# Kernel tuning notes

Hardware: AMD Instinct MI355X
Metric: run time of the kernel (lower is better)

Reference implementation:

```python
import jax, jax.numpy as jnp
from jax import lax
import numpy as np


def _conv(x, w, b):
    y = lax.conv_general_dilated(x, w, (1, 1), 'VALID', dimension_numbers=('NCHW', 'OIHW', 'NCHW'))
    return y + b[None, :, None, None]


def _prelu(x, a):
    return jnp.where(x > 0, x, a[None, :, None, None] * x)


def _pnet(x, c1w, c1b, p1, c2w, c2b, p2, c3w, c3b, p3, w41, b41, w42, b42):
    x = _prelu(_conv(x, c1w, c1b), p1)
    H, W = x.shape[2], x.shape[3]
    # MaxPool2d(2,2, ceil_mode=True): pad bottom/right with -inf when odd
    x = lax.reduce_window(x, -jnp.inf, lax.max, (1, 1, 2, 2), (1, 1, 2, 2),
                          ((0, 0), (0, 0), (0, H % 2), (0, W % 2)))
    x = _prelu(_conv(x, c2w, c2b), p2)
    x = _prelu(_conv(x, c3w, c3b), p3)
    a = jax.nn.softmax(_conv(x, w41, b41), axis=1)
    b = _conv(x, w42, b42)
    return b, a


def _nms(boxes, scores, imgidx, valid, thr):
    # masked, fixed-size batched NMS (per-image via coordinate offset trick)
    N = boxes.shape[0]
    order = jnp.argsort(-jnp.where(valid, scores, -1e9))
    b = boxes[order] + imgidx[order].astype(boxes.dtype)[:, None] * 1e5
    v = valid[order]
    x1, y1, x2, y2 = b[:, 0], b[:, 1], b[:, 2], b[:, 3]
    area = jnp.maximum(x2 - x1, 0.0) * jnp.maximum(y2 - y1, 0.0)
    ar = jnp.arange(N)

    def body(i, keep):
        iw = jnp.maximum(jnp.minimum(x2[i], x2) - jnp.maximum(x1[i], x1), 0.0)
        ih = jnp.maximum(jnp.minimum(y2[i], y2) - jnp.maximum(y1[i], y1), 0.0)
        inter = iw * ih
        iou = inter / (area[i] + area - inter + 1e-9)
        return keep & ~((iou > thr) & (ar > i) & keep[i])

    keep = lax.fori_loop(0, N, body, v)
    return order, keep


def _detect(images, c1w, c1b, p1, c2w, c2b, p2, c3w, c3b, p3, w41, b41, w42, b42):
    params = (c1w, c1b, p1, c2w, c2b, p2, c3w, c3b, p3, w41, b41, w42, b42)
    x = jnp.transpose(images, (0, 3, 1, 2))  # NHWC -> NCHW
    B, _, H, W = x.shape
    m = 12.0 / 20.0  # 12 / minsize
    scales = []
    ml, si = min(H, W) * m, m
    while ml >= 12:
        scales.append(si)
        si *= 0.709
        ml *= 0.709
    KS, THR0 = 512, 0.6  # fixed per-scale candidate capacity
    all_b, all_i, all_k = [], [], []
    for scale in scales:
        nh, nw = int(H * scale + 1), int(W * scale + 1)
        im = jax.image.resize(x, (B, 3, nh, nw), method='linear')
        im = (im - 127.5) * 0.0078125
        reg, label = _pnet(im, *params)
        probs = label[:, 1]  # [B,h,w]
        b_, h_, w_ = probs.shape
        yy, xx = jnp.meshgrid(jnp.arange(h_), jnp.arange(w_), indexing='ij')
        bbx = jnp.tile(xx.reshape(-1), b_).astype(x.dtype)
        bby = jnp.tile(yy.reshape(-1), b_).astype(x.dtype)
        # stride=2, cellsize=12 grid-cell -> image-space boxes
        q = [jnp.floor((2 * bbx + 1) / scale), jnp.floor((2 * bby + 1) / scale),
             jnp.floor((2 * bbx + 12) / scale), jnp.floor((2 * bby + 12) / scale)]
        score = probs.reshape(-1)
        reg4 = jnp.transpose(reg, (0, 2, 3, 1)).reshape(-1, 4)
        boxes9 = jnp.concatenate([jnp.stack(q + [score], axis=1), reg4], axis=1)  # [N,9]
        imgidx = jnp.repeat(jnp.arange(b_), h_ * w_)
        k = min(KS, boxes9.shape[0])
        vals, idx = lax.top_k(jnp.where(score >= THR0, score, -1e9), k)
        bsel, isel, vsel = boxes9[idx], imgidx[idx], vals > -1e8
        order, keep = _nms(bsel[:, :4], bsel[:, 4], isel, vsel, 0.5)
        all_b.append(bsel[order])
        all_i.append(isel[order])
        all_k.append(keep)
    boxes = jnp.concatenate(all_b, 0)
    iidx = jnp.concatenate(all_i, 0)
    kp = jnp.concatenate(all_k, 0)
    K2 = min(1024, boxes.shape[0])
    vals, idx = lax.top_k(jnp.where(kp, boxes[:, 4], -1e9), K2)
    b2, i2, v2 = boxes[idx], iidx[idx], vals > -1e8
    order, keep = _nms(b2[:, :4], b2[:, 4], i2, v2, 0.7)
    b2 = b2[order]
    regw, regh = b2[:, 2] - b2[:, 0], b2[:, 3] - b2[:, 1]
    out = jnp.stack([b2[:, 0] + b2[:, 5] * regw, b2[:, 1] + b2[:, 6] * regh,
                     b2[:, 2] + b2[:, 7] * regw, b2[:, 3] + b2[:, 8] * regh, b2[:, 4]], axis=1)
    # rerec: square-ify
    hh, ww = out[:, 3] - out[:, 1], out[:, 2] - out[:, 0]
    l = jnp.maximum(hh, ww)
    x1 = out[:, 0] + ww * 0.5 - l * 0.5
    y1 = out[:, 1] + hh * 0.5 - l * 0.5
    out = jnp.stack([x1, y1, x1 + l, y1 + l, out[:, 4]], axis=1)
    return out * keep[:, None].astype(out.dtype)  # invalid/suppressed rows zeroed


def setup_inputs():
    key = jax.random.key(0)
    ks = jax.random.split(key, 16)
    rn = lambda k, s, sc=0.1: jax.random.normal(k, s, dtype=jnp.float32) * sc
    return {
        'images': jax.random.uniform(ks[0], (8, 768, 768, 3), dtype=jnp.float32) * 255.0,
        'c1w': rn(ks[1], (10, 3, 3, 3)), 'c1b': rn(ks[2], (10,)),
        'p1': 0.25 * jnp.ones((10,), jnp.float32),
        'c2w': rn(ks[3], (16, 10, 3, 3)), 'c2b': rn(ks[4], (16,)),
        'p2': 0.25 * jnp.ones((16,), jnp.float32),
        'c3w': rn(ks[5], (32, 16, 3, 3)), 'c3b': rn(ks[6], (32,)),
        'p3': 0.25 * jnp.ones((32,), jnp.float32),
        'w41': rn(ks[7], (2, 32, 1, 1)), 'b41': rn(ks[8], (2,)),
        'w42': rn(ks[9], (4, 32, 1, 1)), 'b42': rn(ks[10], (4,)),
    }


def reference(images, c1w, c1b, p1, c2w, c2b, p2, c3w, c3b, p3, w41, b41, w42, b42):
    return _detect(images, c1w, c1b, p1, c2w, c2b, p2, c3w, c3b, p3, w41, b41, w42, b42)
```

## Files before the change

kernel.cpp:

```cpp
#include <hip/hip_runtime.h>
#include <stdint.h>

typedef unsigned long long u64;
typedef unsigned int u32;

#define TPB 256
#define NJMAX 12
#define NSC 11

__device__ __forceinline__ int findJob(const int* cum, int nj, int v) {
  int j = 0;
  while (j + 1 < nj && v >= cum[j + 1]) ++j;
  return j;
}

struct MkP { int ns; int nw[NSC]; float invs[NSC], ks[NSC];
             int oxB[NSC], T[NSC], wOff[NSC]; };

__global__ void k_mkweights(int* __restrict__ tX0, int* __restrict__ tCNT,
                            float* __restrict__ tWT, float* __restrict__ tW, MkP P) {
  const int s = blockIdx.x;
  const int nw = P.nw[s];
  const float invs = P.invs[s], ks = P.ks[s];
  const int T = P.T[s];
  for (int ox = threadIdx.x; ox < nw; ox += TPB) {
    float sx = ((float)ox + 0.5f) * invs - 0.5f;
    int x0 = (int)ceilf(sx - ks); if (x0 < 0) x0 = 0;
    int x1 = (int)floorf(sx + ks); if (x1 > 767) x1 = 767;
    float wt = 0.f;
    float* wv = tW + P.wOff[s];
    for (int j = x0; j <= x1; ++j) {
      float w = fmaxf(0.f, 1.f - fabsf(sx - (float)j) / ks);
      wt += w;
      wv[(j - x0) * nw + ox] = w;
    }
    for (int k = x1 - x0 + 1; k < T; ++k) wv[k * nw + ox] = 0.f;
    int g = P.oxB[s] + ox;
    tX0[g] = x0; tCNT[g] = x1 - x0 + 1; tWT[g] = wt;
  }
}

struct DscP { int nj; int N[NJMAX]; int hOff[NJMAX], imgOff[NJMAX];
              int oxB[NJMAX], wOff[NJMAX];
              int cumW[NJMAX + 1], cumR[NJMAX + 1]; };

__global__ void k_mkdesc(int* __restrict__ hd, int* __restrict__ vd,
                         int hdcap, int vdcap, DscP P) {
  int gid = blockIdx.x * TPB + threadIdx.x;
  int totW = P.cumW[P.nj], totR = P.cumR[P.nj];
  if (gid < totW) {
    int j = findJob(P.cumW, P.nj, gid);
    int local = gid - P.cumW[j];
    int N = P.N[j];
    int ox = local % N, c = local / N;
    hd[gid]             = P.hOff[j] + c * 768 * N + ox;
    hd[hdcap + gid]     = c * 769;
    hd[2 * hdcap + gid] = N;
    hd[3 * hdcap + gid] = P.oxB[j] + ox;
    hd[4 * hdcap + gid] = P.wOff[j] + ox;
  }
  if (gid < totR) {
    int j = findJob(P.cumR, P.nj, gid);
    int local = gid - P.cumR[j];
    int N = P.N[j];
    int oy = local % N, q = local / N;
    vd[gid]             = P.hOff[j] + q * 768 * N;
    vd[vdcap + gid]     = P.imgOff[j] + (q * N + oy) * N;
    vd[2 * vdcap + gid] = P.oxB[j] + oy;
    vd[3 * vdcap + gid] = P.wOff[j] + oy;
    vd[4 * vdcap + gid] = N;
  }
}

__global__ void k_resizeH_d(const float* __restrict__ img, float* __restrict__ base,
                            const int* __restrict__ tX0, const int* __restrict__ tCNT,
                            const float* __restrict__ tWT, const float* __restrict__ tW,
                            const int* __restrict__ hd, int hdcap, int total) {
  __shared__ float row[3][769];
  const int y = blockIdx.x, b = blockIdx.y;
  const float* src = img + ((long)b * 768 + y) * 768 * 3;
  for (int t = threadIdx.x; t < 2304; t += TPB) {
    int x = t / 3, c = t - 3 * x;
    row[c][x] = src[t];
  }
  __syncthreads();
  const float* rowF = &row[0][0];
  const long yb = (long)y + 2304L * b;
  for (int t = threadIdx.x; t < total; t += TPB) {
    int A = hd[t];
    int R = hd[hdcap + t];
    int N = hd[2 * hdcap + t];
    int g = hd[3 * hdcap + t];
    int W = hd[4 * hdcap + t];
    int x0 = tX0[g], cnt = tCNT[g];
    float wt = tWT[g];
    const float* wv = tW + W;
    const float* rp = rowF + R + x0;
    float acc = 0.f;
    int k = 0;
    for (; k + 3 < cnt; k += 4) {
      float v0 = rp[k],     w0 = wv[(long)k * N];
      float v1 = rp[k + 1], w1 = wv[(long)(k + 1) * N];
      float v2 = rp[k + 2], w2 = wv[(long)(k + 2) * N];
      float v3 = rp[k + 3], w3 = wv[(long)(k + 3) * N];
      acc += v0 * w0; acc += v1 * w1; acc += v2 * w2; acc += v3 * w3;
    }
    for (; k < cnt; ++k) acc += rp[k] * wv[(long)k * N];
    base[(long)A + (long)N * yb] = acc / wt;
  }
}

__global__ void k_resizeV_row(const float* __restrict__ basep, float* __restrict__ img,
                              const int* __restrict__ tX0, const int* __restrict__ tCNT,
                              const float* __restrict__ tWT, const float* __restrict__ tW,
                              const int* __restrict__ vd, int vdcap, int nRows) {
  int row = blockIdx.x * 4 + (threadIdx.x >> 6);
  if (row >= nRows) return;
  int lane = threadIdx.x & 63;
  int S = vd[row];
  int O = vd[vdcap + row];
  int g = vd[2 * vdcap + row];
  int W = vd[3 * vdcap + row];
  int N = vd[4 * vdcap + row];
  int y0 = tX0[g], cnt = tCNT[g];
  float wt = tWT[g];
  const float* wv = tW + W;
  const float* col0 = basep + S + (long)y0 * N;
  for (int ox = lane; ox < N; ox += 64) {
    const float* col = col0 + ox;
    float acc = 0.f;
    int k = 0;
    for (; k + 3 < cnt; k += 4) {
      float v0 = col[(long)k * N],       w0 = wv[(long)k * N];
      float v1 = col[(long)(k + 1) * N], w1 = wv[(long)(k + 1) * N];
      float v2 = col[(long)(k + 2) * N], w2 = wv[(long)(k + 2) * N];
      float v3 = col[(long)(k + 3) * N], w3 = wv[(long)(k + 3) * N];
      acc += v0 * w0; acc += v1 * w1; acc += v2 * w2; acc += v3 * w3;
    }
    for (; k < cnt; ++k) acc += col[(long)k * N] * wv[(long)k * N];
    img[(long)O + ox] = (acc / wt - 127.5f) * 0.0078125f;
  }
}

__device__ __forceinline__ void conv1pool_body(
    const float* in, const float* w, const float* bias, const float* pr,
    float* out, int H, int W, int b, int px, int py) {
  const int h1 = H - 2, w1 = W - 2;
  const int PH = (h1 + 1) >> 1, PW = (w1 + 1) >> 1;
  if (px >= PW || py >= PH) return;
  const int x0 = px * 2, y0 = py * 2;
  float a00[10], a01[10], a10[10], a11[10];
#pragma unroll
  for (int co = 0; co < 10; ++co) { a00[co] = 0.f; a01[co] = 0.f; a10[co] = 0.f; a11[co] = 0.f; }
  const long HW = (long)H * W;
  const float* pp = in + ((long)b * 3 * H + y0) * W + x0;
  for (int ci = 0; ci < 3; ++ci, pp += HW) {
    const float* r = pp;
    float r00 = r[0], r01 = r[1], r02 = r[2], r03 = r[3]; r += W;
    float r10 = r[0], r11 = r[1], r12 = r[2], r13 = r[3]; r += W;
    float r20 = r[0], r21 = r[1], r22 = r[2], r23 = r[3]; r += W;
    float r30 = r[0], r31 = r[1], r32 = r[2], r33 = r[3];
#pragma unroll
    for (int co = 0; co < 10; ++co) {
      const float* wc = w + ((long)co * 3 + ci) * 9;
      float w0 = wc[0], w1_ = wc[1], w2 = wc[2];
      float w3 = wc[3], w4 = wc[4], w5 = wc[5];
      float w6 = wc[6], w7 = wc[7], w8 = wc[8];
      a00[co] += r00 * w0 + r01 * w1_ + r02 * w2;
      a00[co] += r10 * w3 + r11 * w4 + r12 * w5;
      a00[co] += r20 * w6 + r21 * w7 + r22 * w8;
      a01[co] += r01 * w0 + r02 * w1_ + r03 * w2;
      a01[co] += r11 * w3 + r12 * w4 + r13 * w5;
      a01[co] += r21 * w6 + r22 * w7 + r23 * w8;
      a10[co] += r10 * w0 + r11 * w1_ + r12 * w2;
      a10[co] += r20 * w3 + r21 * w4 + r22 * w5;
      a10[co] += r30 * w6 + r31 * w7 + r32 * w8;
      a11[co] += r11 * w0 + r12 * w1_ + r13 * w2;
      a11[co] += r21 * w3 + r22 * w4 + r23 * w5;
      a11[co] += r31 * w6 + r32 * w7 + r33 * w8;
    }
  }
  const bool vx = (x0 + 1 < w1), vy = (y0 + 1 < h1);
#pragma unroll
  for (int co = 0; co < 10; ++co) {
    const float bb = bias[co], al = pr[co];
    float v = a00[co] + bb; v = v > 0.f ? v : al * v;
    float m = v;
    if (vx) { v = a01[co] + bb; v = v > 0.f ? v : al * v; m = fmaxf(m, v); }
    if (vy) { v = a10[co] + bb; v = v > 0.f ? v : al * v; m = fmaxf(m, v); }
    if (vx && vy) { v = a11[co] + bb; v = v > 0.f ? v : al * v; m = fmaxf(m, v); }
    out[(((long)b * 10 + co) * PH + py) * PW + px] = m;
  }
}

struct C1P { int nj; int nh[NJMAX]; int imgOff[NJMAX], poolOff[NJMAX];
             int t1x[NJMAX]; int cumT[NJMAX + 1]; };

__global__ void k_conv1pool_job(const float* __restrict__ imgb, const float* __restrict__ w,
                                const float* __restrict__ bias, const float* __restrict__ pr,
                                float* __restrict__ poolb, C1P P) {
  int j = findJob(P.cumT, P.nj, blockIdx.x);
  int local = blockIdx.x - P.cumT[j];
  int t1x = P.t1x[j];
  int tX = local % t1x, tY = local / t1x;
  conv1pool_body(imgb + P.imgOff[j], w, bias, pr, poolb + P.poolOff[j],
                 P.nh[j], P.nh[j], blockIdx.z,
                 tX * 16 + (threadIdx.x & 15), tY * 16 + (threadIdx.x >> 4));
}

__device__ __forceinline__ void conv3x3c8_body(
    const float* in, const float* w, const float* bias, const float* pr,
    float* out, int Cin, int Cout, int H, int W, int cog, int b, int x0, int y) {
  const int OH = H - 2, OW = W - 2;
  if (y >= OH || x0 >= OW) return;
  float acc[8][4];
#pragma unroll
  for (int k = 0; k < 8; ++k) { acc[k][0] = 0.f; acc[k][1] = 0.f; acc[k][2] = 0.f; acc[k][3] = 0.f; }
  const float* wp = w + (long)cog * Cin * 9;
  const long HW = (long)H * W;
  const float* pp = in + ((long)b * Cin * H + y) * W + x0;
  for (int ci = 0; ci < Cin; ++ci, pp += HW) {
    const float* r = pp;
    float q00 = r[0], q01 = r[1], q02 = r[2], q03 = r[3], q04 = r[4], q05 = r[5]; r += W;
    float q10 = r[0], q11 = r[1], q12 = r[2], q13 = r[3], q14 = r[4], q15 = r[5]; r += W;
    float q20 = r[0], q21 = r[1], q22 = r[2], q23 = r[3], q24 = r[4], q25 = r[5];
#pragma unroll
    for (int k = 0; k < 8; ++k) {
      const float* wc = wp + ((long)k * Cin + ci) * 9;
      float w0 = wc[0], w1 = wc[1], w2 = wc[2];
      float w3 = wc[3], w4 = wc[4], w5 = wc[5];
      float w6 = wc[6], w7 = wc[7], w8 = wc[8];
      acc[k][0] += q00 * w0 + q01 * w1 + q02 * w2;
      acc[k][1] += q01 * w0 + q02 * w1 + q03 * w2;
      acc[k][2] += q02 * w0 + q03 * w1 + q04 * w2;
      acc[k][3] += q03 * w0 + q04 * w1 + q05 * w2;
      acc[k][0] += q10 * w3 + q11 * w4 + q12 * w5;
      acc[k][1] += q11 * w3 + q12 * w4 + q13 * w5;
      acc[k][2] += q12 * w3 + q13 * w4 + q14 * w5;
      acc[k][3] += q13 * w3 + q14 * w4 + q15 * w5;
      acc[k][0] += q20 * w6 + q21 * w7 + q22 * w8;
      acc[k][1] += q21 * w6 + q22 * w7 + q23 * w8;
      acc[k][2] += q22 * w6 + q23 * w7 + q24 * w8;
      acc[k][3] += q23 * w6 + q24 * w7 + q25 * w8;
    }
  }
  const int rem = OW - x0;
#pragma unroll
  for (int k = 0; k < 8; ++k) {
    const int co = cog + k;
    const float bb = bias[co], al = pr[co];
    float* op = out + (((long)b * Cout + co) * OH + y) * OW + x0;
    float v0 = acc[k][0] + bb; v0 = v0 > 0.f ? v0 : al * v0;
    op[0] = v0;
    if (rem > 1) { float v = acc[k][1] + bb; v = v > 0.f ? v : al * v; op[1] = v; }
    if (rem > 2) { float v = acc[k][2] + bb; v = v > 0.f ? v : al * v; op[2] = v; }
    if (rem > 3) { float v = acc[k][3] + bb; v = v > 0.f ? v : al * v; op[3] = v; }
  }
}

struct CvP { int nj; int H[NJMAX]; int inOff[NJMAX], outOff[NJMAX];
             int tx[NJMAX]; int cumT[NJMAX + 1]; };

__global__ void k_conv3x3c8_job(const float* __restrict__ inb, const float* __restrict__ w,
                                const float* __restrict__ bias, const float* __restrict__ pr,
                                float* __restrict__ outb, int Cin, int Cout, CvP P) {
  int j = findJob(P.cumT, P.nj, blockIdx.x);
  int local = blockIdx.x - P.cumT[j];
  int tx0 = P.tx[j];
  int tX = local % tx0, tY = local / tx0;
  conv3x3c8_body(inb + P.inOff[j], w, bias, pr, outb + P.outOff[j], Cin, Cout,
                 P.H[j], P.H[j], blockIdx.y * 8, blockIdx.z,
                 tX * 64 + (threadIdx.x & 15) * 4, tY * 16 + (threadIdx.x >> 4));
}

__device__ __forceinline__ void head_body(const float* x3, const float* w41,
                                          const float* b41, const float* w42,
                                          const float* b42, float* reg, u64* keys,
                                          int plane, long idx) {
  int b = (int)(idx / plane); int rem = (int)(idx % plane);
  const float* p = x3 + (long)b * 32 * plane + rem;
  float l0 = 0.f, l1 = 0.f, r0 = 0.f, r1 = 0.f, r2 = 0.f, r3 = 0.f;
  for (int c = 0; c < 32; ++c) {
    float v = p[(long)c * plane];
    l0 += v * w41[c];      l1 += v * w41[32 + c];
    r0 += v * w42[c];      r1 += v * w42[32 + c];
    r2 += v * w42[64 + c]; r3 += v * w42[96 + c];
  }
  l0 += b41[0]; l1 += b41[1];
  r0 += b42[0]; r1 += b42[1]; r2 += b42[2]; r3 += b42[3];
  float mx = fmaxf(l0, l1);
  float e0 = expf(l0 - mx), e1 = expf(l1 - mx);
  float s = e1 / (e0 + e1);
  reg[idx * 4 + 0] = r0; reg[idx * 4 + 1] = r1;
  reg[idx * 4 + 2] = r2; reg[idx * 4 + 3] = r3;
  u32 ic = 0xFFFFFFFFu - (u32)idx;
  u64 k = (s >= 0.6f) ? ((((u64)__float_as_uint(s)) << 32) | ic) : (u64)ic;
  keys[idx] = k;
}

struct HdP { int nj; int h3[NJMAX]; int c3Off[NJMAX], kOff[NJMAX];
             int cumC[NJMAX + 1]; };

__global__ void k_head_job(const float* __restrict__ c3b, const float* __restrict__ w41,
                           const float* __restrict__ b41, const float* __restrict__ w42,
                           const float* __restrict__ b42, float* __restrict__ regb,
                           u64* __restrict__ keysb, HdP P) {
  int gid = blockIdx.x * TPB + threadIdx.x;
  if (gid >= P.cumC[P.nj]) return;
  int j = findJob(P.cumC, P.nj, gid);
  int idx = gid - P.cumC[j];
  head_body(c3b + P.c3Off[j], w41, b41, w42, b42,
            regb + 4L * P.kOff[j], keysb + P.kOff[j], P.h3[j] * P.h3[j], idx);
}

__device__ __forceinline__ void bitonic2048(u64* s) {
  for (int k = 2; k <= 2048; k <<= 1) {
    for (int j = k >> 1; j > 0; j >>= 1) {
      for (int i = threadIdx.x; i < 2048; i += TPB) {
        int ixj = i ^ j;
        if (ixj > i) {
          u64 a = s[i], b = s[ixj];
          bool desc = ((i & k) == 0);
          if (desc ? (a < b) : (a > b)) { s[i] = b; s[ixj] = a; }
        }
      }
      __syncthreads();
    }
  }
}

struct TkP { int nj; int srcSel[NJMAX]; int srcOff[NJMAX]; int n[NJMAX];
             int dstOff[NJMAX]; int cumB[NJMAX + 1]; };

__global__ void k_topk_job(u64* __restrict__ A, u64* __restrict__ B, TkP P) {
  __shared__ u64 s[2048];
  int j = findJob(P.cumB, P.nj, blockIdx.x);
  int lb = blockIdx.x - P.cumB[j];
  const u64* src = (P.srcSel[j] ? B : A) + P.srcOff[j];
  u64* dst = (P.srcSel[j] ? A : B) + P.dstOff[j];
  int n = P.n[j];
  int base = lb * 2048;
  for (int t = threadIdx.x; t < 2048; t += TPB) {
    int gi = base + t;
    s[t] = (gi < n) ? src[gi] : 0ULL;
  }
  __syncthreads();
  bitonic2048(s);
  for (int t = threadIdx.x; t < 512; t += TPB)
    dst[(long)lb * 512 + t] = s[t];
}

struct TkFP { int nj; int srcSel[NJMAX]; int srcOff[NJMAX]; int n[NJMAX]; int sIdx[NJMAX]; };

__global__ void k_topk_fin(const u64* __restrict__ A, const u64* __restrict__ B,
                           u64* __restrict__ selk, TkFP P) {
  __shared__ u64 s[2048];
  int j = blockIdx.x;
  const u64* src = (P.srcSel[j] ? B : A) + P.srcOff[j];
  int n = P.n[j];
  for (int t = threadIdx.x; t < 2048; t += TPB)
    s[t] = (t < n) ? src[t] : 0ULL;
  __syncthreads();
  bitonic2048(s);
  for (int t = threadIdx.x; t < 512; t += TPB)
    selk[(long)P.sIdx[j] * 512 + t] = s[t];
}

__device__ __forceinline__ void gather_body(const u64* keys, const float* reg,
                                            float* boxes, int h, int w, float scalef,
                                            int i) {
  float* bx = boxes + (long)i * 12;
  u64 key = keys[i];
  if ((key >> 32) == 0ULL) {
    for (int q = 0; q < 12; ++q) bx[q] = 0.f;
    return;
  }
  u32 cell = 0xFFFFFFFFu - (u32)(key & 0xFFFFFFFFu);
  int x = (int)(cell % (u32)w); u32 t2 = cell / (u32)w;
  int y = (int)(t2 % (u32)h); int b = (int)(t2 / (u32)h);
  float fx = (float)x, fy = (float)y;
  bx[0] = floorf((2.f * fx + 1.f) / scalef);
  bx[1] = floorf((2.f * fy + 1.f) / scalef);
  bx[2] = floorf((2.f * fx + 12.f) / scalef);
  bx[3] = floorf((2.f * fy + 12.f) / scalef);
  bx[4] = __uint_as_float((u32)(key >> 32));
  bx[5] = reg[(long)cell * 4 + 0];
  bx[6] = reg[(long)cell * 4 + 1];
  bx[7] = reg[(long)cell * 4 + 2];
  bx[8] = reg[(long)cell * 4 + 3];
  bx[9] = (float)b;
  bx[10] = 1.f;
  bx[11] = 0.f;
}

struct GtP { int nj; int h3[NJMAX]; float scalef[NJMAX]; int kOff[NJMAX]; int sIdx[NJMAX]; };

__global__ void k_gather_job(const u64* __restrict__ selk, const float* __restrict__ regb,
                             float* __restrict__ boxes, GtP P) {
  int j = blockIdx.x >> 1;
  int i = ((blockIdx.x & 1) << 8) + threadIdx.x;
  gather_body(selk + (long)P.sIdx[j] * 512, regb + 4L * P.kOff[j],
              boxes + (long)P.sIdx[j] * 512 * 12, P.h3[j], P.h3[j], P.scalef[j], i);
}

__global__ void k_nms(float* __restrict__ boxes, int per, float thr) {
  __shared__ float sx1[1024], sy1[1024], sx2[1024], sy2[1024], sar[1024];
  __shared__ unsigned char kp[1024];
  __shared__ unsigned char kb[64];
  __shared__ int snv;
  float* bs = boxes + (long)blockIdx.x * per * 12;
  int N = per;
  if (threadIdx.x == 0) snv = 0;
  __syncthreads();
  for (int i = threadIdx.x; i < N; i += blockDim.x) {
    const float* b = bs + (long)i * 12;
    float off = b[9] * 100000.0f;
    float a0 = b[0] + off, a1 = b[1] + off, a2 = b[2] + off, a3 = b[3] + off;
    sx1[i] = a0; sy1[i] = a1; sx2[i] = a2; sy2[i] = a3;
    sar[i] = fmaxf(a2 - a0, 0.f) * fmaxf(a3 - a1, 0.f);
    bool v = (b[10] != 0.f);
    kp[i] = v;
    if (v) atomicMax(&snv, i + 1);
  }
  __syncthreads();
  int nv = snv;
  const int wave = threadIdx.x >> 6, lane = threadIdx.x & 63;
  for (int base = 0; base < nv; base += 64) {
    const int lim = (nv - base < 64) ? (nv - base) : 64;
    if (wave == 0) {
      int gi = base + lane;
      bool ok = (lane < lim) && kp[gi];
      float bx1 = 0.f, by1 = 0.f, bx2 = 0.f, by2 = 0.f, ba = 0.f;
      if (lane < lim) { bx1 = sx1[gi]; by1 = sy1[gi]; bx2 = sx2[gi]; by2 = sy2[gi]; ba = sar[gi]; }
      for (int i = 0; i < lim; ++i) {
        int ki = __shfl((int)ok, i);
        float xi1 = __shfl(bx1, i), yi1 = __shfl(by1, i);
        float xi2 = __shfl(bx2, i), yi2 = __shfl(by2, i);
        float ai = __shfl(ba, i);
        if (ki && lane > i && ok) {
          float iw = fmaxf(fminf(xi2, bx2) - fmaxf(xi1, bx1), 0.f);
          float ih = fmaxf(fminf(yi2, by2) - fmaxf(yi1, by1), 0.f);
          float inter = iw * ih;
          float iou = inter / (ai + ba - inter + 1e-9f);
          if (iou > thr) ok = false;
        }
      }
      if (lane < lim) kp[gi] = ok ? 1 : 0;
      kb[lane] = (lane < lim && ok) ? 1 : 0;
    }
    __syncthreads();
    for (int j = base + 64 + threadIdx.x; j < nv; j += blockDim.x) {
      if (!kp[j]) continue;
      float jx2 = sx2[j], jy2 = sy2[j], jx1 = sx1[j], jy1 = sy1[j], ja = sar[j];
      bool ok = true;
      for (int i = 0; i < lim && ok; ++i) {
        if (!kb[i]) continue;
        int gi = base + i;
        float iw = fmaxf(fminf(sx2[gi], jx2) - fmaxf(sx1[gi], jx1), 0.f);
        float ih = fmaxf(fminf(sy2[gi], jy2) - fmaxf(sy1[gi], jy1), 0.f);
        float inter = iw * ih;
        float iou = inter / (sar[gi] + ja - inter + 1e-9f);
        if (iou > thr) ok = false;
      }
      if (!ok) kp[j] = 0;
    }
    __syncthreads();
  }
  for (int i = threadIdx.x; i < N; i += blockDim.x)
    bs[(long)i * 12 + 11] = kp[i] ? 1.f : 0.f;
}

__global__ void k_final(const float* __restrict__ boxes, int total, float thr,
                        float* __restrict__ selfb, float* __restrict__ out) {
  __shared__ u64 s[8192];
  __shared__ unsigned char kb[64];
  __shared__ int snv;
  float* fb = (float*)s;
  const int tid = threadIdx.x;
  for (int i = tid; i < 8192; i += 1024) {
    u64 k = 0ULL;
    if (i < total) {
      const float* b = boxes + (long)i * 12;
      u32 ic = 0xFFFFFFFFu - (u32)i;
      k = (b[11] != 0.f) ? ((((u64)__float_as_uint(b[4])) << 32) | ic) : (u64)ic;
    }
    s[i] = k;
  }
  if (tid == 0) snv = 0;
  __syncthreads();
  for (int k = 2; k <= 8192; k <<= 1) {
    for (int j = k >> 1; j > 0; j >>= 1) {
      for (int i = tid; i < 8192; i += 1024) {
        int ixj = i ^ j;
        if (ixj > i) {
          u64 a = s[i], b = s[ixj];
          bool desc = ((i & k) == 0);
          if (desc ? (a < b) : (a > b)) { s[i] = b; s[ixj] = a; }
        }
      }
      __syncthreads();
    }
  }
  u64 myKey = s[tid];
  __syncthreads();
  float* sx1 = fb;
  float* sy1 = fb + 1024;
  float* sx2 = fb + 2048;
  float* sy2 = fb + 3072;
  float* sar = fb + 4096;
  unsigned char* kp = (unsigned char*)(fb + 5120);
  {
    int i = tid;
    float* o = selfb + (long)i * 12;
    if ((myKey >> 32) == 0ULL) {
      for (int q = 0; q < 12; ++q) o[q] = 0.f;
      sx1[i] = 0.f; sy1[i] = 0.f; sx2[i] = 0.f; sy2[i] = 0.f; sar[i] = 0.f;
      kp[i] = 0;
    } else {
      u32 bi = 0xFFFFFFFFu - (u32)(myKey & 0xFFFFFFFFu);
      const float* b = boxes + (long)bi * 12;
      float r0 = b[0], r1 = b[1], r2 = b[2], r3 = b[3], r4 = b[4];
      float r5 = b[5], r6 = b[6], r7 = b[7], r8 = b[8], r9 = b[9];
      o[0] = r0; o[1] = r1; o[2] = r2; o[3] = r3; o[4] = r4;
      o[5] = r5; o[6] = r6; o[7] = r7; o[8] = r8; o[9] = r9;
      o[10] = 1.f; o[11] = 0.f;
      float off = r9 * 100000.0f;
      float a0 = r0 + off, a1 = r1 + off, a2 = r2 + off, a3 = r3 + off;
      sx1[i] = a0; sy1[i] = a1; sx2[i] = a2; sy2[i] = a3;
      sar[i] = fmaxf(a2 - a0, 0.f) * fmaxf(a3 - a1, 0.f);
      kp[i] = 1;
      atomicMax(&snv, i + 1);
    }
  }
  __syncthreads();
  int nv = snv;
  const int wave = tid >> 6, lane = tid & 63;
  for (int base = 0; base < nv; base += 64) {
    const int lim = (nv - base < 64) ? (nv - base) : 64;
    if (wave == 0) {
      int gi = base + lane;
      bool ok = (lane < lim) && kp[gi];
      float bx1 = 0.f, by1 = 0.f, bx2 = 0.f, by2 = 0.f, ba = 0.f;
      if (lane < lim) { bx1 = sx1[gi]; by1 = sy1[gi]; bx2 = sx2[gi]; by2 = sy2[gi]; ba = sar[gi]; }
      for (int i = 0; i < lim; ++i) {
        int ki = __shfl((int)ok, i);
        float xi1 = __shfl(bx1, i), yi1 = __shfl(by1, i);
        float xi2 = __shfl(bx2, i), yi2 = __shfl(by2, i);
        float ai = __shfl(ba, i);
        if (ki && lane > i && ok) {
          float iw = fmaxf(fminf(xi2, bx2) - fmaxf(xi1, bx1), 0.f);
          float ih = fmaxf(fminf(yi2, by2) - fmaxf(yi1, by1), 0.f);
          float inter = iw * ih;
          float iou = inter / (ai + ba - inter + 1e-9f);
          if (iou > thr) ok = false;
        }
      }
      if (lane < lim) kp[gi] = ok ? 1 : 0;
      kb[lane] = (lane < lim && ok) ? 1 : 0;
    }
    __syncthreads();
    for (int j = base + 64 + tid; j < nv; j += blockDim.x) {
      if (!kp[j]) continue;
      float jx2 = sx2[j], jy2 = sy2[j], jx1 = sx1[j], jy1 = sy1[j], ja = sar[j];
      bool ok = true;
      for (int i = 0; i < lim && ok; ++i) {
        if (!kb[i]) continue;
        int gi = base + i;
        float iw = fmaxf(fminf(sx2[gi], jx2) - fmaxf(sx1[gi], jx1), 0.f);
        float ih = fmaxf(fminf(sy2[gi], jy2) - fmaxf(sy1[gi], jy1), 0.f);
        float inter = iw * ih;
        float iou = inter / (sar[gi] + ja - inter + 1e-9f);
        if (iou > thr) ok = false;
      }
      if (!ok) kp[j] = 0;
    }
    __syncthreads();
  }
  {
    int i = tid;
    const float* b = selfb + (long)i * 12;
    float keep = kp[i] ? 1.f : 0.f;
    float x1 = b[0], y1 = b[1], x2 = b[2], y2 = b[3], sc = b[4];
    float rw = x2 - x1, rh = y2 - y1;
    float o0 = x1 + b[5] * rw;
    float o1 = y1 + b[6] * rh;
    float o2 = x2 + b[7] * rw;
    float o3 = y2 + b[8] * rh;
    float hh = o3 - o1, ww = o2 - o0;
    float l = fmaxf(hh, ww);
    float nx1 = o0 + ww * 0.5f - l * 0.5f;
    float ny1 = o1 + hh * 0.5f - l * 0.5f;
    out[(long)i * 5 + 0] = nx1 * keep;
    out[(long)i * 5 + 1] = ny1 * keep;
    out[(long)i * 5 + 2] = (nx1 + l) * keep;
    out[(long)i * 5 + 3] = (ny1 + l) * keep;
    out[(long)i * 5 + 4] = sc * keep;
  }
}

extern "C" void kernel_launch(void* const* d_in, const int* in_sizes, int n_in,
                              void* d_out, int out_size, void* d_ws, size_t ws_size,
                              hipStream_t stream) {
  (void)in_sizes; (void)n_in; (void)out_size;
  const float* images = (const float*)d_in[0];
  const float* c1w = (const float*)d_in[1];
  const float* c1b = (const float*)d_in[2];
  const float* p1  = (const float*)d_in[3];
  const float* c2w = (const float*)d_in[4];
  const float* c2b = (const float*)d_in[5];
  const float* p2  = (const float*)d_in[6];
  const float* c3w = (const float*)d_in[7];
  const float* c3b = (const float*)d_in[8];
  const float* p3  = (const float*)d_in[9];
  const float* w41 = (const float*)d_in[10];
  const float* b41 = (const float*)d_in[11];
  const float* w42 = (const float*)d_in[12];
  const float* b42 = (const float*)d_in[13];
  float* ws = (float*)d_ws;

  double scl[16]; int nsc = 0;
  {
    double m = 12.0 / 20.0;
    double ml = 768.0 * m;
    double si = m;
    while (ml >= 12.0) { scl[nsc++] = si; si *= 0.709; ml *= 0.709; }
  }

  auto cdiv = [](long a, long b) { return (int)((a + b - 1) / b); };

  int NH[NSC], PH_[NSC], H2[NSC], H3[NSC], OXB[NSC], TT[NSC], WOFF[NSC];
  float INV[NSC], KSF[NSC];
  {
    int oxb = 0, woff = 0;
    for (int s = 0; s < nsc; ++s) {
      int nh = (int)(768.0 * scl[s] + 1.0);
      NH[s] = nh;
      PH_[s] = ((nh - 2) + 1) / 2;
      H2[s] = PH_[s] - 2;
      H3[s] = H2[s] - 2;
      double inv = 1.0 / (((double)nh) / 768.0);
      INV[s] = (float)inv;
      KSF[s] = (float)(inv > 1.0 ? inv : 1.0);
      TT[s] = (int)(2.0f * KSF[s]) + 2;
      OXB[s] = oxb; oxb += nh;
      WOFF[s] = woff; woff += nh * TT[s];
    }
  }

  static const int GA[11] = {0, 1, 2, 3, 4, 5, 6, 7, 8, 9, 10};
  static const int G1[7] = {0, 5, 6, 7, 8, 9, 10};
  static const int G2[4] = {1, 2, 3, 4};

  struct Layout {
    long HT, IMG, POOL, C2, REG, KEYS, SCR, SEL, BOX, FK, FS, SF, TBL, HD, VD, extent;
    int hdcap, vdcap;
  };

  auto calcLayout = [&](const int* const* gps, const int* gn, int ng,
                        int hdcap, int vdcap, Layout& L) {
    long htA = 0, c3A = 0, imgA = 0, poolA = 0, c2A = 0, cellsA = 0, scrA = 0;
    for (int g = 0; g < ng; ++g) {
      long ht = 0, c3 = 0, im = 0, pl = 0, c2s = 0, ck = 0, sc = 0;
      for (int q = 0; q < gn[g]; ++q) {
        int s = gps[g][q];
        ht += 24L * 768 * NH[s];
        im += 24L * NH[s] * NH[s];
        pl += 80L * PH_[s] * PH_[s];
        c2s += 128L * H2[s] * H2[s];
        c3 += 256L * H3[s] * H3[s];
        long cells = 8L * H3[s] * H3[s];
        ck += cells;
        sc += 512L * ((cells + 2047) / 2048);
      }
      if (ht > htA) htA = ht; if (c3 > c3A) c3A = c3; if (im > imgA) imgA = im;
      if (pl > poolA) poolA = pl; if (c2s > c2A) c2A = c2s;
      if (ck > cellsA) cellsA = ck; if (sc > scrA) scrA = sc;
    }
    long htR = htA > c3A ? htA : c3A;
    auto al = [](long v) { return (v + 15) & ~15L; };
    long off = 0;
    L.HT = off;   off += al(htR);
    L.IMG = off;  off += al(imgA);
    L.POOL = off; off += al(poolA);
    L.C2 = off;   off += al(c2A);
    L.REG = off;  off += al(4 * cellsA);
    L.KEYS = off; off += al(2 * cellsA);
    L.SCR = off;  off += al(2 * scrA + 16384);
    L.SEL = off;  off += al(11264);
    L.BOX = off;  off += al(67584);
    L.FK = off;   off += al(16384);
    L.FS = off;   off += al(2048);
    L.SF = off;   off += al(12288);
    L.TBL = off;  off += al(12288 + 24000);
    L.HD = off;   off += al((long)ng * 5 * hdcap);
    L.VD = off;   off += al((long)ng * 5 * vdcap);
    L.extent = off;
    L.hdcap = hdcap; L.vdcap = vdcap;
  };

  Layout LA, LB;
  {
    const int* gpsA[1] = {GA}; int gnA[1] = {11};
    calcLayout(gpsA, gnA, 1, 8192, 56320, LA);
    const int* gpsB[2] = {G1, G2}; int gnB[2] = {7, 4};
    calcLayout(gpsB, gnB, 2, 2560, 20480, LB);
  }
  bool big = (ws_size >= (size_t)LA.extent * 4);
  const Layout& L = big ? LA : LB;
  const int* GS[2]; int GN[2]; int ngroups;
  if (big) { GS[0] = GA; GN[0] = 11; ngroups = 1; }
  else { GS[0] = G1; GN[0] = 7; GS[1] = G2; GN[1] = 4; ngroups = 2; }

  u64* keys  = (u64*)(ws + L.KEYS);
  u64* scr   = (u64*)(ws + L.SCR);
  u64* selk  = (u64*)(ws + L.SEL);
  float* boxes = ws + L.BOX;
  float* self  = ws + L.SF;
  int*   tX0  = (int*)(ws + L.TBL);
  int*   tCNT = (int*)(ws + L.TBL + 4096);
  float* tWT  = ws + L.TBL + 8192;
  float* tW   = ws + L.TBL + 12288;

  {
    MkP P; P.ns = nsc;
    for (int s = 0; s < nsc; ++s) {
      P.nw[s] = NH[s]; P.invs[s] = INV[s]; P.ks[s] = KSF[s];
      P.oxB[s] = OXB[s]; P.T[s] = TT[s]; P.wOff[s] = WOFF[s];
    }
    k_mkweights<<<nsc, TPB, 0, stream>>>(tX0, tCNT, tWT, tW, P);
  }

  int imgOff[2][NJMAX], poolOff[2][NJMAX], c2Off[2][NJMAX], c3Off[2][NJMAX],
      htOff[2][NJMAX], kOff[2][NJMAX], cells[2][NJMAX];
  int cumWtot[2], cumRtot[2];
  for (int g = 0; g < ngroups; ++g) {
    long ch = 0, ci = 0, cp = 0, c2 = 0, c3 = 0, ck = 0;
    int cw = 0, cr = 0;
    for (int q = 0; q < GN[g]; ++q) {
      int s = GS[g][q];
      htOff[g][q] = (int)ch;  ch += 24L * 768 * NH[s];
      imgOff[g][q] = (int)ci; ci += 24L * NH[s] * NH[s];
      poolOff[g][q] = (int)cp; cp += 80L * PH_[s] * PH_[s];
      c2Off[g][q] = (int)c2;  c2 += 128L * H2[s] * H2[s];
      c3Off[g][q] = (int)c3;  c3 += 256L * H3[s] * H3[s];
      kOff[g][q] = (int)ck;   cells[g][q] = 8 * H3[s] * H3[s]; ck += cells[g][q];
      cw += 3 * NH[s]; cr += 24 * NH[s];
    }
    cumWtot[g] = cw; cumRtot[g] = cr;
  }

  for (int g = 0; g < ngroups; ++g) {
    DscP P; P.nj = GN[g];
    int cw = 0, cr = 0;
    for (int q = 0; q < GN[g]; ++q) {
      int s = GS[g][q];
      P.N[q] = NH[s]; P.hOff[q] = htOff[g][q]; P.imgOff[q] = imgOff[g][q];
      P.oxB[q] = OXB[s]; P.wOff[q] = WOFF[s];
      P.cumW[q] = cw; cw += 3 * NH[s];
      P.cumR[q] = cr; cr += 24 * NH[s];
    }
    P.cumW[GN[g]] = cw; P.cumR[GN[g]] = cr;
    int* hd = (int*)(ws + L.HD) + (long)g * 5 * L.hdcap;
    int* vd = (int*)(ws + L.VD) + (long)g * 5 * L.vdcap;
    int tot = cw > cr ? cw : cr;
    k_mkdesc<<<cdiv(tot, TPB), TPB, 0, stream>>>(hd, vd, L.hdcap, L.vdcap, P);
  }

  for (int g = 0; g < ngroups; ++g) {
    const int* gs = GS[g];
    int nj = GN[g];
    int* hd = (int*)(ws + L.HD) + (long)g * 5 * L.hdcap;
    int* vd = (int*)(ws + L.VD) + (long)g * 5 * L.vdcap;
    {
      dim3 gh(768, 8, 1);
      k_resizeH_d<<<gh, TPB, 0, stream>>>(images, ws + L.HT, tX0, tCNT, tWT, tW,
                                          hd, L.hdcap, cumWtot[g]);
    }
    k_resizeV_row<<<cdiv(cumRtot[g], 4), TPB, 0, stream>>>(
        ws + L.HT, ws + L.IMG, tX0, tCNT, tWT, tW, vd, L.vdcap, cumRtot[g]);
    {
      C1P P; P.nj = nj; int ct = 0;
      for (int q = 0; q < nj; ++q) {
        int s = gs[q];
        P.nh[q] = NH[s];
        P.imgOff[q] = imgOff[g][q]; P.poolOff[q] = poolOff[g][q];
        int t1x = cdiv(PH_[s], 16);
        P.t1x[q] = t1x;
        P.cumT[q] = ct; ct += t1x * t1x;
      }
      P.cumT[nj] = ct;
      dim3 gg(ct, 1, 8);
      k_conv1pool_job<<<gg, TPB, 0, stream>>>(ws + L.IMG, c1w, c1b, p1, ws + L.POOL, P);
    }
    {
      CvP P; P.nj = nj; int ct = 0;
      for (int q = 0; q < nj; ++q) {
        int s = gs[q];
        P.H[q] = PH_[s];
        P.inOff[q] = poolOff[g][q]; P.outOff[q] = c2Off[g][q];
        int tx = cdiv(H2[s], 64), ty = cdiv(H2[s], 16);
        P.tx[q] = tx;
        P.cumT[q] = ct; ct += tx * ty;
      }
      P.cumT[nj] = ct;
      dim3 gg(ct, 2, 8);
      k_conv3x3c8_job<<<gg, TPB, 0, stream>>>(ws + L.POOL, c2w, c2b, p2, ws + L.C2,
                                              10, 16, P);
    }
    {
      CvP P; P.nj = nj; int ct = 0;
      for (int q = 0; q < nj; ++q) {
        int s = gs[q];
        P.H[q] = H2[s];
        P.inOff[q] = c2Off[g][q]; P.outOff[q] = c3Off[g][q];
        int tx = cdiv(H3[s], 64), ty = cdiv(H3[s], 16);
        P.tx[q] = tx;
        P.cumT[q] = ct; ct += tx * ty;
      }
      P.cumT[nj] = ct;
      dim3 gg(ct, 4, 8);
      k_conv3x3c8_job<<<gg, TPB, 0, stream>>>(ws + L.C2, c3w, c3b, p3, ws + L.HT,
                                              16, 32, P);
    }
    {
      HdP P; P.nj = nj; int cc = 0;
      for (int q = 0; q < nj; ++q) {
        int s = gs[q];
        P.h3[q] = H3[s];
        P.c3Off[q] = c3Off[g][q]; P.kOff[q] = kOff[g][q];
        P.cumC[q] = cc; cc += cells[g][q];
      }
      P.cumC[nj] = cc;
      k_head_job<<<cdiv(cc, TPB), TPB, 0, stream>>>(ws + L.HT, w41, b41, w42, b42,
                                                    ws + L.REG, keys, P);
    }
    {
      int bOff[NJMAX];
      {
        int c = 0;
        for (int q = 0; q < nj; ++q) { bOff[q] = c; c += 512 * cdiv(cells[g][q], 2048); }
      }
      long nCur[NJMAX]; int par[NJMAX];
      for (int q = 0; q < nj; ++q) { nCur[q] = cells[g][q]; par[q] = 0; }
      while (true) {
        TkP P; P.nj = 0; int cum = 0; int act[NJMAX];
        for (int q = 0; q < nj; ++q) {
          if (nCur[q] > 2048) {
            int r = P.nj++;
            act[r] = q;
            int blocks = cdiv(nCur[q], 2048);
            P.srcSel[r] = par[q];
            P.srcOff[r] = par[q] ? bOff[q] : kOff[g][q];
            P.dstOff[r] = par[q] ? kOff[g][q] : bOff[q];
            P.n[r] = (int)nCur[q];
            P.cumB[r] = cum; cum += blocks;
          }
        }
        P.cumB[P.nj] = cum;
        if (P.nj == 0) break;
        k_topk_job<<<cum, TPB, 0, stream>>>(keys, scr, P);
        for (int r = 0; r < P.nj; ++r) {
          int q = act[r];
          nCur[q] = 512L * cdiv(nCur[q], 2048);
          par[q] ^= 1;
        }
      }
      TkFP F; F.nj = nj;
      for (int q = 0; q < nj; ++q) {
        F.srcSel[q] = par[q];
        F.srcOff[q] = par[q] ? bOff[q] : kOff[g][q];
        F.n[q] = (int)nCur[q];
        F.sIdx[q] = gs[q];
      }
      k_topk_fin<<<nj, TPB, 0, stream>>>(keys, scr, selk, F);
    }
    {
      GtP P; P.nj = nj;
      for (int q = 0; q < nj; ++q) {
        int s = gs[q];
        P.h3[q] = H3[s]; P.scalef[q] = (float)scl[s]; P.kOff[q] = kOff[g][q];
        P.sIdx[q] = s;
      }
      k_gather_job<<<2 * nj, TPB, 0, stream>>>(selk, ws + L.REG, boxes, P);
    }
  }

  k_nms<<<nsc, TPB, 0, stream>>>(boxes, 512, 0.5f);

  int total = nsc * 512;
  k_final<<<1, 1024, 0, stream>>>(boxes, total, 0.7f, self, (float*)d_out);
}
```

Baseline: 998.5 us.

## Fuse final top-k, box gather and per-scale NMS; widen top-k reduction blocks

The final per-scale top-k sort, the box gather and the per-scale NMS are merged into one kernel that keeps the selected keys and box coordinates in shared memory, so the selk buffer round-trip and two launches go away. The multi-pass top-k reduction now sorts 8192-element tiles with 1024-thread blocks instead of 2048-element tiles, which cuts the number of reduction passes and launches. The larger bitonic sort does more work per block and uses 64KB of shared memory, which may reduce occupancy.

```diff
diff --git a/kernel.cpp b/kernel.cpp
--- a/kernel.cpp
+++ b/kernel.cpp
@@ -332,95 +332,91 @@
 struct TkP { int nj; int srcSel[NJMAX]; int srcOff[NJMAX]; int n[NJMAX];
              int dstOff[NJMAX]; int cumB[NJMAX + 1]; };
 
-__global__ void k_topk_job(u64* __restrict__ A, u64* __restrict__ B, TkP P) {
-  __shared__ u64 s[2048];
+__global__ __launch_bounds__(1024) void k_topk_job8(u64* __restrict__ A,
+                                                    u64* __restrict__ B, TkP P) {
+  __shared__ u64 s[8192];
   int j = findJob(P.cumB, P.nj, blockIdx.x);
   int lb = blockIdx.x - P.cumB[j];
   const u64* src = (P.srcSel[j] ? B : A) + P.srcOff[j];
   u64* dst = (P.srcSel[j] ? A : B) + P.dstOff[j];
   int n = P.n[j];
-  int base = lb * 2048;
-  for (int t = threadIdx.x; t < 2048; t += TPB) {
+  int base = lb * 8192;
+  for (int t = threadIdx.x; t < 8192; t += 1024) {
     int gi = base + t;
     s[t] = (gi < n) ? src[gi] : 0ULL;
   }
   __syncthreads();
-  bitonic2048(s);
-  for (int t = threadIdx.x; t < 512; t += TPB)
+  for (int k = 2; k <= 8192; k <<= 1) {
+    for (int jj = k >> 1; jj > 0; jj >>= 1) {
+      for (int i = threadIdx.x; i < 8192; i += 1024) {
+        int ixj = i ^ jj;
+        if (ixj > i) {
+          u64 a = s[i], b = s[ixj];
+          bool desc = ((i & k) == 0);
+          if (desc ? (a < b) : (a > b)) { s[i] = b; s[ixj] = a; }
+        }
+      }
+      __syncthreads();
+    }
+  }
+  for (int t = threadIdx.x; t < 512; t += 1024)
     dst[(long)lb * 512 + t] = s[t];
 }
 
-struct TkFP { int nj; int srcSel[NJMAX]; int srcOff[NJMAX]; int n[NJMAX]; int sIdx[NJMAX]; };
-
-__global__ void k_topk_fin(const u64* __restrict__ A, const u64* __restrict__ B,
-                           u64* __restrict__ selk, TkFP P) {
+struct TlP { int nj; int srcSel[NJMAX]; int srcOff[NJMAX]; int n[NJMAX];
+             int sIdx[NJMAX]; int h3[NJMAX]; float scalef[NJMAX]; int kOff[NJMAX]; };
+
+__global__ void k_tail(const u64* __restrict__ A, const u64* __restrict__ B,
+                       const float* __restrict__ regb, float* __restrict__ boxes,
+                       float thr, TlP P) {
   __shared__ u64 s[2048];
-  int j = blockIdx.x;
+  __shared__ float sx1[512], sy1[512], sx2[512], sy2[512], sar[512];
+  __shared__ unsigned char kp[512];
+  __shared__ unsigned char kb[64];
+  __shared__ int snv;
+  const int j = blockIdx.x;
   const u64* src = (P.srcSel[j] ? B : A) + P.srcOff[j];
   int n = P.n[j];
   for (int t = threadIdx.x; t < 2048; t += TPB)
     s[t] = (t < n) ? src[t] : 0ULL;
+  if (threadIdx.x == 0) snv = 0;
   __syncthreads();
   bitonic2048(s);
-  for (int t = threadIdx.x; t < 512; t += TPB)
-    selk[(long)P.sIdx[j] * 512 + t] = s[t];
-}
-
-__device__ __forceinline__ void gather_body(const u64* keys, const float* reg,
-                                            float* boxes, int h, int w, float scalef,
-                                            int i) {
-  float* bx = boxes + (long)i * 12;
-  u64 key = keys[i];
-  if ((key >> 32) == 0ULL) {
-    for (int q = 0; q < 12; ++q) bx[q] = 0.f;
-    return;
-  }
-  u32 cell = 0xFFFFFFFFu - (u32)(key & 0xFFFFFFFFu);
-  int x = (int)(cell % (u32)w); u32 t2 = cell / (u32)w;
-  int y = (int)(t2 % (u32)h); int b = (int)(t2 / (u32)h);
-  float fx = (float)x, fy = (float)y;
-  bx[0] = floorf((2.f * fx + 1.f) / scalef);
-  bx[1] = floorf((2.f * fy + 1.f) / scalef);
-  bx[2] = floorf((2.f * fx + 12.f) / scalef);
-  bx[3] = floorf((2.f * fy + 12.f) / scalef);
-  bx[4] = __uint_as_float((u32)(key >> 32));
-  bx[5] = reg[(long)cell * 4 + 0];
-  bx[6] = reg[(long)cell * 4 + 1];
-  bx[7] = reg[(long)cell * 4 + 2];
-  bx[8] = reg[(long)cell * 4 + 3];
-  bx[9] = (float)b;
-  bx[10] = 1.f;
-  bx[11] = 0.f;
-}
-
-struct GtP { int nj; int h3[NJMAX]; float scalef[NJMAX]; int kOff[NJMAX]; int sIdx[NJMAX]; };
-
-__global__ void k_gather_job(const u64* __restrict__ selk, const float* __restrict__ regb,
-                             float* __restrict__ boxes, GtP P) {
-  int j = blockIdx.x >> 1;
-  int i = ((blockIdx.x & 1) << 8) + threadIdx.x;
-  gather_body(selk + (long)P.sIdx[j] * 512, regb + 4L * P.kOff[j],
-              boxes + (long)P.sIdx[j] * 512 * 12, P.h3[j], P.h3[j], P.scalef[j], i);
-}
-
-__global__ void k_nms(float* __restrict__ boxes, int per, float thr) {
-  __shared__ float sx1[1024], sy1[1024], sx2[1024], sy2[1024], sar[1024];
-  __shared__ unsigned char kp[1024];
-  __shared__ unsigned char kb[64];
-  __shared__ int snv;
-  float* bs = boxes + (long)blockIdx.x * per * 12;
-  int N = per;
-  if (threadIdx.x == 0) snv = 0;
-  __syncthreads();
-  for (int i = threadIdx.x; i < N; i += blockDim.x) {
-    const float* b = bs + (long)i * 12;
-    float off = b[9] * 100000.0f;
-    float a0 = b[0] + off, a1 = b[1] + off, a2 = b[2] + off, a3 = b[3] + off;
-    sx1[i] = a0; sy1[i] = a1; sx2[i] = a2; sy2[i] = a3;
-    sar[i] = fmaxf(a2 - a0, 0.f) * fmaxf(a3 - a1, 0.f);
-    bool v = (b[10] != 0.f);
-    kp[i] = v;
-    if (v) atomicMax(&snv, i + 1);
+  float* bset = boxes + (long)P.sIdx[j] * 512 * 12;
+  const int h = P.h3[j];
+  const float scalef = P.scalef[j];
+  const float* reg = regb + 4L * P.kOff[j];
+  for (int i = threadIdx.x; i < 512; i += TPB) {
+    u64 key = s[i];
+    float* bx = bset + (long)i * 12;
+    if ((key >> 32) == 0ULL) {
+      for (int q = 0; q < 12; ++q) bx[q] = 0.f;
+      sx1[i] = 0.f; sy1[i] = 0.f; sx2[i] = 0.f; sy2[i] = 0.f; sar[i] = 0.f;
+      kp[i] = 0;
+    } else {
+      u32 cell = 0xFFFFFFFFu - (u32)(key & 0xFFFFFFFFu);
+      int x = (int)(cell % (u32)h); u32 t2 = cell / (u32)h;
+      int y = (int)(t2 % (u32)h); int b = (int)(t2 / (u32)h);
+      float fx = (float)x, fy = (float)y;
+      float b0 = floorf((2.f * fx + 1.f) / scalef);
+      float b1 = floorf((2.f * fy + 1.f) / scalef);
+      float b2 = floorf((2.f * fx + 12.f) / scalef);
+      float b3 = floorf((2.f * fy + 12.f) / scalef);
+      float b4 = __uint_as_float((u32)(key >> 32));
+      float b9 = (float)b;
+      bx[0] = b0; bx[1] = b1; bx[2] = b2; bx[3] = b3; bx[4] = b4;
+      bx[5] = reg[(long)cell * 4 + 0];
+      bx[6] = reg[(long)cell * 4 + 1];
+      bx[7] = reg[(long)cell * 4 + 2];
+      bx[8] = reg[(long)cell * 4 + 3];
+      bx[9] = b9; bx[10] = 1.f; bx[11] = 0.f;
+      float off = b9 * 100000.0f;
+      float a0 = b0 + off, a1 = b1 + off, a2 = b2 + off, a3 = b3 + off;
+      sx1[i] = a0; sy1[i] = a1; sx2[i] = a2; sy2[i] = a3;
+      sar[i] = fmaxf(a2 - a0, 0.f) * fmaxf(a3 - a1, 0.f);
+      kp[i] = 1;
+      atomicMax(&snv, i + 1);
+    }
   }
   __syncthreads();
   int nv = snv;
@@ -449,9 +445,9 @@
       kb[lane] = (lane < lim && ok) ? 1 : 0;
     }
     __syncthreads();
-    for (int j = base + 64 + threadIdx.x; j < nv; j += blockDim.x) {
-      if (!kp[j]) continue;
-      float jx2 = sx2[j], jy2 = sy2[j], jx1 = sx1[j], jy1 = sy1[j], ja = sar[j];
+    for (int jj = base + 64 + threadIdx.x; jj < nv; jj += blockDim.x) {
+      if (!kp[jj]) continue;
+      float jx2 = sx2[jj], jy2 = sy2[jj], jx1 = sx1[jj], jy1 = sy1[jj], ja = sar[jj];
       bool ok = true;
       for (int i = 0; i < lim && ok; ++i) {
         if (!kb[i]) continue;
@@ -462,12 +458,12 @@
         float iou = inter / (sar[gi] + ja - inter + 1e-9f);
         if (iou > thr) ok = false;
       }
-      if (!ok) kp[j] = 0;
+      if (!ok) kp[jj] = 0;
     }
     __syncthreads();
   }
-  for (int i = threadIdx.x; i < N; i += blockDim.x)
-    bs[(long)i * 12 + 11] = kp[i] ? 1.f : 0.f;
+  for (int i = threadIdx.x; i < 512; i += TPB)
+    bset[(long)i * 12 + 11] = kp[i] ? 1.f : 0.f;
 }
 
 __global__ void k_final(const float* __restrict__ boxes, int total, float thr,
@@ -713,7 +709,6 @@
 
   u64* keys  = (u64*)(ws + L.KEYS);
   u64* scr   = (u64*)(ws + L.SCR);
-  u64* selk  = (u64*)(ws + L.SEL);
   float* boxes = ws + L.BOX;
   float* self  = ws + L.SF;
   int*   tX0  = (int*)(ws + L.TBL);
@@ -838,7 +833,7 @@
       int bOff[NJMAX];
       {
         int c = 0;
-        for (int q = 0; q < nj; ++q) { bOff[q] = c; c += 512 * cdiv(cells[g][q], 2048); }
+        for (int q = 0; q < nj; ++q) { bOff[q] = c; c += 512 * cdiv(cells[g][q], 8192); }
       }
       long nCur[NJMAX]; int par[NJMAX];
       for (int q = 0; q < nj; ++q) { nCur[q] = cells[g][q]; par[q] = 0; }
@@ -848,7 +843,7 @@
           if (nCur[q] > 2048) {
             int r = P.nj++;
             act[r] = q;
-            int blocks = cdiv(nCur[q], 2048);
+            int blocks = cdiv(nCur[q], 8192);
             P.srcSel[r] = par[q];
             P.srcOff[r] = par[q] ? bOff[q] : kOff[g][q];
             P.dstOff[r] = par[q] ? kOff[g][q] : bOff[q];
@@ -858,34 +853,27 @@
         }
         P.cumB[P.nj] = cum;
         if (P.nj == 0) break;
-        k_topk_job<<<cum, TPB, 0, stream>>>(keys, scr, P);
+        k_topk_job8<<<cum, 1024, 0, stream>>>(keys, scr, P);
         for (int r = 0; r < P.nj; ++r) {
           int q = act[r];
-          nCur[q] = 512L * cdiv(nCur[q], 2048);
+          nCur[q] = 512L * cdiv(nCur[q], 8192);
           par[q] ^= 1;
         }
       }
-      TkFP F; F.nj = nj;
+      TlP F; F.nj = nj;
       for (int q = 0; q < nj; ++q) {
+        int s = gs[q];
         F.srcSel[q] = par[q];
         F.srcOff[q] = par[q] ? bOff[q] : kOff[g][q];
         F.n[q] = (int)nCur[q];
-        F.sIdx[q] = gs[q];
-      }
-      k_topk_fin<<<nj, TPB, 0, stream>>>(keys, scr, selk, F);
-    }
-    {
-      GtP P; P.nj = nj;
-      for (int q = 0; q < nj; ++q) {
-        int s = gs[q];
-        P.h3[q] = H3[s]; P.scalef[q] = (float)scl[s]; P.kOff[q] = kOff[g][q];
-        P.sIdx[q] = s;
-      }
-      k_gather_job<<<2 * nj, TPB, 0, stream>>>(selk, ws + L.REG, boxes, P);
-    }
-  }
-
-  k_nms<<<nsc, TPB, 0, stream>>>(boxes, 512, 0.5f);
+        F.sIdx[q] = s;
+        F.h3[q] = H3[s];
+        F.scalef[q] = (float)scl[s];
+        F.kOff[q] = kOff[g][q];
+      }
+      k_tail<<<nj, TPB, 0, stream>>>(keys, scr, ws + L.REG, boxes, 0.5f, F);
+    }
+  }
 
   int total = nsc * 512;
   k_final<<<1, 1024, 0, stream>>>(boxes, total, 0.7f, self, (float*)d_out);
```

Result: faster. 944.6 us (median of 2 runs) (-5.4%).
